# Kernel tuning notes

Hardware: AMD Instinct MI355X
Metric: run time of the kernel (lower is better)

Reference implementation:

```python
import jax, jax.numpy as jnp
import numpy as np

N, E, G = 50000, 150000, 200
D, ED_IN, EH = 320, 15, 32
NB, NT = 3, 9  # conv blocks, edge types


def setup_inputs() -> dict:
    key = jax.random.key(0)
    ks = jax.random.split(key, 16)
    s = 0.02
    return {
        "x": jax.random.normal(ks[0], (N, D), jnp.float32),
        "batch": jnp.sort(jax.random.randint(ks[1], (N,), 0, G)),
        "edge_indices": jax.random.randint(ks[2], (NT, 2, E), 0, N),
        "edge_attrs": jax.random.normal(ks[3], (NT, E, ED_IN), jnp.float32),
        "W1": jax.random.normal(ks[4], (2 * D + ED_IN, EH), jnp.float32) * s,
        "b1": jnp.zeros((EH,), jnp.float32),
        "W2": jax.random.normal(ks[5], (EH, EH), jnp.float32) * s,
        "b2": jnp.zeros((EH,), jnp.float32),
        "Wq": jax.random.normal(ks[6], (NB, NT, D, D), jnp.float32) * s,
        "bq": jnp.zeros((NB, NT, D), jnp.float32),
        "Wk": jax.random.normal(ks[7], (NB, NT, D, D), jnp.float32) * s,
        "bk": jnp.zeros((NB, NT, D), jnp.float32),
        "Wv": jax.random.normal(ks[8], (NB, NT, D, D), jnp.float32) * s,
        "bv": jnp.zeros((NB, NT, D), jnp.float32),
        "We": jax.random.normal(ks[9], (NB, NT, EH, D), jnp.float32) * s,
        "be": jnp.zeros((NB, NT, D), jnp.float32),
        "Ws": jax.random.normal(ks[10], (NB, NT, D, D), jnp.float32) * s,
        "bs": jnp.zeros((NB, NT, D), jnp.float32),
        "gamma": jnp.ones((NB, D), jnp.float32),
        "beta": jnp.zeros((NB, D), jnp.float32),
    }


def _transformer_conv(x, src, dst, ea, Wq, bq, Wk, bk, Wv, bv, We, be, Ws, bs):
    # PyG TransformerConv, heads=1, edge_dim=EH, eval mode (no dropout).
    q = (x @ Wq + bq)[dst]                    # [E, D] query at destination
    e = ea @ We + be                          # [E, D] projected edge attr
    k = (x @ Wk + bk)[src] + e                # [E, D]
    v = (x @ Wv + bv)[src] + e                # [E, D]
    alpha = (q * k).sum(-1) / jnp.sqrt(jnp.float32(D))  # [E]
    amax = jax.ops.segment_max(alpha, dst, num_segments=N)
    amax = jnp.where(jnp.isfinite(amax), amax, 0.0)     # guard empty segments
    ex = jnp.exp(alpha - amax[dst])
    denom = jax.ops.segment_sum(ex, dst, num_segments=N)
    w = ex / (denom[dst] + 1e-16)
    out = jax.ops.segment_sum(w[:, None] * v, dst, num_segments=N)
    return out + x @ Ws + bs                  # root/skip connection


def _graph_layer_norm(x, batch, gamma, beta):
    # PyG gnn.norm.LayerNorm, mode='graph': normalize per graph over nodes+channels.
    cnt = jax.ops.segment_sum(jnp.ones((N,), x.dtype), batch, num_segments=G)
    norm = jnp.maximum(cnt, 1.0) * D          # elements per graph
    mean = jax.ops.segment_sum(x.sum(-1), batch, num_segments=G) / norm
    xc = x - mean[batch][:, None]
    var = jax.ops.segment_sum((xc * xc).sum(-1), batch, num_segments=G) / norm
    out = xc / jnp.sqrt(var + 1e-5)[batch][:, None]
    return out * gamma + beta


def reference(x, batch, edge_indices, edge_attrs, W1, b1, W2, b2,
              Wq, bq, Wk, bk, Wv, bv, We, be, Ws, bs, gamma, beta):
    # Edge MLP preprocessing (uses original node features x).
    new_ea = []
    for t in range(NT):
        src, dst = edge_indices[t, 0], edge_indices[t, 1]
        cat = jnp.concatenate([x[src], x[dst], edge_attrs[t]], axis=-1)  # [E, 655]
        h = jax.nn.leaky_relu(cat @ W1 + b1)
        new_ea.append(h @ W2 + b2)

    h = x
    for b in range(NB):
        acc = jnp.zeros_like(h)
        for t in range(NT):
            src, dst = edge_indices[t, 0], edge_indices[t, 1]
            acc = acc + _transformer_conv(
                h, src, dst, new_ea[t],
                Wq[b, t], bq[b, t], Wk[b, t], bk[b, t], Wv[b, t], bv[b, t],
                We[b, t], be[b, t], Ws[b, t], bs[b, t])
        x_ = jax.nn.leaky_relu(acc / 9.0)
        x_ = _graph_layer_norm(x_, batch, gamma[b], beta[b])
        h = 0.5 * (h + x_)

    return jax.ops.segment_max(h, batch, num_segments=G)  # global max pool [G, D]
```

## Files before the change

### kernel.cpp

```cpp
#include <hip/hip_runtime.h>

#define N_NODES 50000
#define N_EDGE  150000
#define N_GRAPH 200
#define DIM     320
#define EDI     15
#define EH      32
#define NBLK    3
#define NTYP    9
#define NPAD    51200
#define BPT     50
#define QLD     360
#define QCOLS   353
#define NPQ     384
#define BIGCH   448

typedef unsigned short u16;
typedef unsigned int   u32;
typedef __bf16 bf16x8 __attribute__((ext_vector_type(8)));
typedef float  f32x4  __attribute__((ext_vector_type(4)));

__device__ __forceinline__ float b2f(u16 s) {
    u32 u = ((u32)s) << 16;
    return __builtin_bit_cast(float, u);
}
__device__ __forceinline__ float b2f_lo(u32 u) { return __builtin_bit_cast(float, u << 16); }
__device__ __forceinline__ float b2f_hi(u32 u) { return __builtin_bit_cast(float, u & 0xffff0000u); }
__device__ __forceinline__ u16 f2b(float f) {
    u32 u = __builtin_bit_cast(u32, f);
    u = (u + 0x7fffu + ((u >> 16) & 1u)) >> 16;
    return (u16)u;
}

__device__ __forceinline__ void gll16(const u16* g, u32 ldsAddr) {
    u32 m0v = (u32)__builtin_amdgcn_readfirstlane((int)ldsAddr);
    asm volatile("s_mov_b32 m0, %0\n\t"
                 "global_load_lds_dwordx4 %1, off"
                 :: "s"(m0v), "v"((unsigned long long)(size_t)g)
                 : "memory");
}

__global__ __launch_bounds__(256) void gemm_kernel(
    const u16* __restrict__ A, int Mstride,
    const u16* __restrict__ Bst, const float* __restrict__ bias,
    u16* __restrict__ Cb, float* __restrict__ Cf,
    int ldc, int out_cols, int M, int NP, int KQ, int mode,
    int zA, int zB, int zC)
{
    A += (size_t)blockIdx.z * zA;
    Bst += (size_t)blockIdx.z * zB;
    if (Cb) Cb += (size_t)blockIdx.z * zC;
    if (Cf) Cf += (size_t)blockIdx.z * zC;

    const int tid = threadIdx.x;
    const int wave = tid >> 6, lane = tid & 63;

    const int nwg = gridDim.x * gridDim.y;
    const int flat = blockIdx.y * gridDim.x + blockIdx.x;
    const int qq = nwg >> 3, rr = nwg & 7;
    const int xcd = flat & 7, loc = flat >> 3;
    const int swz = (xcd < rr ? xcd * (qq + 1) : rr * (qq + 1) + (xcd - rr) * qq) + loc;
    const int n0 = (swz % gridDim.x) * 128, m0 = (swz / gridDim.x) * 128;

    const int wm = (wave & 1) << 6, wn = (wave >> 1) << 6;
    const int lm = lane & 15, quad = lane >> 4;

    __shared__ uint4 smem[3][2][512];
    const u32 ldsBase = (u32)(size_t)&smem[0][0][0];

    f32x4 acc[4][4] = {};
    const int nIter = KQ >> 2;

    auto stage = [&](int s, int buf) {
        const int c0 = s << 2;
        const u32 bufBase = ldsBase + (u32)buf * 16384u;
#pragma unroll
        for (int u = 0; u < 2; ++u) {
            const int i = wave + (u << 2);
            const int chunk = i >> 1, half = (i & 1) << 6;
            const u16* ga = A + ((size_t)(c0 + chunk) * Mstride + m0 + half + lane) * 8;
            gll16(ga, bufBase + (u32)i * 1024u);
            const u16* gb = Bst + ((size_t)(c0 + chunk) * NP + n0 + half + lane) * 8;
            gll16(gb, bufBase + 8192u + (u32)i * 1024u);
        }
    };

    stage(0, 0);
    if (nIter > 1) {
        stage(1, 1);
        asm volatile("s_waitcnt vmcnt(4)" ::: "memory");
    } else {
        asm volatile("s_waitcnt vmcnt(0)" ::: "memory");
    }
    __syncthreads();

    int bRd = 0, bIss = 2;
    for (int s = 0; s < nIter; ++s) {
        const bool more = (s + 2 < nIter);
        if (more) { stage(s + 2, bIss); bIss = (bIss == 2) ? 0 : bIss + 1; }
        const uint4* aT = &smem[bRd][0][0];
        const uint4* bT = &smem[bRd][1][0];
        bf16x8 af[4], bfr[4];
#pragma unroll
        for (int mi = 0; mi < 4; ++mi)
            af[mi] = __builtin_bit_cast(bf16x8, aT[quad * 128 + wm + mi * 16 + lm]);
#pragma unroll
        for (int ni = 0; ni < 4; ++ni)
            bfr[ni] = __builtin_bit_cast(bf16x8, bT[quad * 128 + wn + ni * 16 + lm]);
#pragma unroll
        for (int mi = 0; mi < 4; ++mi)
#pragma unroll
            for (int ni = 0; ni < 4; ++ni)
                acc[mi][ni] = __builtin_amdgcn_mfma_f32_16x16x32_bf16(af[mi], bfr[ni], acc[mi][ni], 0, 0, 0);
        if (s + 1 < nIter) {
            if (more) asm volatile("s_waitcnt vmcnt(4)" ::: "memory");
            else      asm volatile("s_waitcnt vmcnt(0)" ::: "memory");
            __syncthreads();
        }
        bRd = (bRd == 2) ? 0 : bRd + 1;
    }

#pragma unroll
    for (int mi = 0; mi < 4; ++mi) {
        int row = m0 + wm + mi * 16 + quad * 4;
#pragma unroll
        for (int ni = 0; ni < 4; ++ni) {
            int col = n0 + wn + ni * 16 + lm;
            float bv = bias ? bias[col] : 0.f;
#pragma unroll
            for (int r = 0; r < 4; ++r) {
                int rr2 = row + r;
                if (rr2 < M && col < out_cols) {
                    float v = acc[mi][ni][r] + bv;
                    size_t off = (size_t)rr2 * ldc + col;
                    if (mode == 0)      Cb[off] = f2b(v);
                    else if (mode == 1) Cf[off] = v;
                    else                Cf[off] += v;
                }
            }
        }
    }
}

__global__ void k_convert_x(const float* __restrict__ x, u16* __restrict__ hb,
                            u16* __restrict__ hNode) {
    int i = blockIdx.x * 256 + threadIdx.x;
    if (i >= N_NODES * DIM) return;
    int node = i / DIM, c = i - node * DIM;
    u16 v = f2b(x[i]);
    hb[((size_t)(c >> 3) * N_NODES + node) * 8 + (c & 7)] = v;
    hNode[i] = v;
}

__global__ void k_prep_wT(const float* __restrict__ W, u16* __restrict__ T) {
    int i = blockIdx.x * 256 + threadIdx.x;
    if (i >= 27 * 40 * 320) return;
    int e = i % 320, jq = (i / 320) % 40, bt = i / (320 * 40);
    const float* src = W + ((size_t)bt * 320 + e) * 320 + jq * 8;
    u16 tmp[8];
#pragma unroll
    for (int r = 0; r < 8; ++r) tmp[r] = f2b(src[r]);
    *(uint4*)(&T[(((size_t)bt * 40 + jq) * 320 + e) * 8]) = *(uint4*)tmp;
}

__global__ void k_prep_qkvW(const u16* __restrict__ Mb, u16* __restrict__ Bst) {
    int i = blockIdx.x * 256 + threadIdx.x;
    if (i >= 27 * 40 * NPQ) return;
    int col = i % NPQ, kq = (i / NPQ) % 40, bt = i / (NPQ * 40);
    if (col >= 320 && col < QCOLS) return;
    u16 tmp[8];
    if (col >= QCOLS) {
#pragma unroll
        for (int r = 0; r < 8; ++r) tmp[r] = 0;
    } else {
#pragma unroll
        for (int r = 0; r < 8; ++r)
            tmp[r] = Mb[((size_t)bt * 320 + kq * 8 + r) * 320 + col];
    }
    *(uint4*)(&Bst[(((size_t)bt * 40 + kq) * NPQ + col) * 8]) = *(uint4*)tmp;
}

__global__ __launch_bounds__(256) void k_prep_ext(
    const float* __restrict__ Wq, const float* __restrict__ bq,
    const float* __restrict__ We, const float* __restrict__ be,
    const float* __restrict__ bk,
    u16* __restrict__ Bst, float* __restrict__ biasQkv)
{
    __shared__ float WeL[33 * 321];
    int bt = blockIdx.x, kt = blockIdx.y;
    for (int i = threadIdx.x; i < 33 * 320; i += 256) {
        int r = i / 320, d = i - r * 320;
        WeL[r * 321 + d] = (r < 32) ? We[((size_t)bt * 32 + r) * 320 + d]
                                    : (be[(size_t)bt * 320 + d] + bk[(size_t)bt * 320 + d]);
    }
    __syncthreads();
    if (kt < 10) {
        int k  = kt * 32 + (threadIdx.x >> 3);
        int ct = threadIdx.x & 7;
        const float* wq = Wq + ((size_t)bt * 320 + k) * 320;
        float dot[5] = {0.f, 0.f, 0.f, 0.f, 0.f};
        for (int d = 0; d < 320; ++d) {
            float w = wq[d];
            dot[0] += w * WeL[ct * 321 + d];
            dot[1] += w * WeL[(ct + 8) * 321 + d];
            dot[2] += w * WeL[(ct + 16) * 321 + d];
            dot[3] += w * WeL[(ct + 24) * 321 + d];
            dot[4] += w * WeL[32 * 321 + d];
        }
#pragma unroll
        for (int u = 0; u < 4; ++u)
            Bst[(((size_t)bt * 40 + (k >> 3)) * NPQ + 320 + ct + u * 8) * 8 + (k & 7)] = f2b(dot[u]);
        if (ct == 0)
            Bst[(((size_t)bt * 40 + (k >> 3)) * NPQ + 352) * 8 + (k & 7)] = f2b(dot[4]);
    } else {
        int c = threadIdx.x;
        if (c < 33) {
            const float* b = bq + (size_t)bt * 320;
            float s = 0.f;
            for (int d = 0; d < 320; ++d) s += b[d] * WeL[c * 321 + d];
            biasQkv[bt * NPQ + 320 + c] = s;
        }
    }
}

__global__ __launch_bounds__(256) void k_prep_qkvB(
    const float* __restrict__ Wk, const float* __restrict__ bq,
    float* __restrict__ bias)
{
    int i = blockIdx.x * 256 + threadIdx.x;
    if (i >= 27 * NPQ) return;
    int col = i % NPQ, bt = i / NPQ;
    if (col < 320) {
        const float4* wr = (const float4*)(Wk + ((size_t)bt * 320 + col) * 320);
        const float4* bb = (const float4*)(bq + (size_t)bt * 320);
        float s = 0.f;
        for (int j = 0; j < 80; ++j) {
            float4 a = wr[j], b = bb[j];
            s += a.x * b.x + a.y * b.y + a.z * b.z + a.w * b.w;
        }
        bias[bt * NPQ + col] = s;
    } else if (col >= QCOLS) {
        bias[bt * NPQ + col] = 0.f;
    }
}

__global__ void k_prep_skipB(const float* __restrict__ bs, float* __restrict__ bias) {
    int i = blockIdx.x * 256 + threadIdx.x;
    if (i >= 3 * 384) return;
    int col = i % 384, b = i / 384;
    float v = 0.f;
    if (col < 320)
        for (int t = 0; t < 9; ++t) v += bs[(b * 9 + t) * 320 + col];
    bias[i] = v;
}

__global__ void k_prep_bigB(const float* __restrict__ Ws, const float* __restrict__ Wv,
                            const float* __restrict__ We, const float* __restrict__ be,
                            const float* __restrict__ bv, u16* __restrict__ Bst) {
    int i = blockIdx.x * 256 + threadIdx.x;
    if (i >= 3 * BIGCH * 384) return;
    int col = i % 384, q = (i / 384) % BIGCH, b = i / (384 * BIGCH);
    u16 tmp[8];
#pragma unroll
    for (int r = 0; r < 8; ++r) {
        int k = q * 8 + r;
        float v = 0.f;
        if (col < 320) {
            if (k < 320) {
                for (int t = 0; t < 9; ++t)
                    v += Ws[((size_t)(b * 9 + t) * 320 + k) * 320 + col];
            } else {
                int kk = k - 320, t = kk / 360, kl = kk - t * 360;
                if (t < 9) {
                    int bt = b * 9 + t;
                    if (kl < 320)       v = Wv[((size_t)bt * 320 + kl) * 320 + col];
                    else if (kl < 352)  v = We[((size_t)bt * 32 + (kl - 320)) * 320 + col];
                    else if (kl == 352) v = be[(size_t)bt * 320 + col] + bv[(size_t)bt * 320 + col];
                }
            }
        }
        tmp[r] = f2b(v);
    }
    *(uint4*)(&Bst[(((size_t)b * BIGCH + q) * 384 + col) * 8]) = *(uint4*)tmp;
}

__global__ void k_prep_w1W(const float* __restrict__ W1, u16* __restrict__ Bst) {
    int i = blockIdx.x * 256 + threadIdx.x;
    if (i >= 320 * 128) return;
    int col = i & 127, k = i >> 7;
    float v = 0.f;
    if (col < 32)      v = W1[(size_t)k * 32 + col];
    else if (col < 64) v = W1[(size_t)(320 + k) * 32 + (col - 32)];
    Bst[((size_t)(k >> 3) * 128 + col) * 8 + (k & 7)] = f2b(v);
}

__global__ void k_csr_zero(int* __restrict__ cnt) {
    int i = blockIdx.x * 256 + threadIdx.x;
    if (i < NTYP * NPAD) cnt[i] = 0;
}
__global__ void k_csr_count(const int* __restrict__ eidx, int* __restrict__ cnt) {
    int i = blockIdx.x * 256 + threadIdx.x;
    if (i >= NTYP * N_EDGE) return;
    int t = i / N_EDGE, e = i - t * N_EDGE;
    int dst = eidx[(size_t)(t * 2 + 1) * N_EDGE + e];
    atomicAdd(&cnt[t * NPAD + dst], 1);
}
__global__ __launch_bounds__(1024) void k_csr_scan1(const int* __restrict__ cnt,
                                                    int* __restrict__ rowStart,
                                                    int* __restrict__ blockSum) {
    __shared__ int tmp[1024];
    int t = blockIdx.y, blk = blockIdx.x, tid = threadIdx.x;
    int idx = t * NPAD + blk * 1024 + tid;
    int v = cnt[idx];
    tmp[tid] = v;
    __syncthreads();
    for (int off = 1; off < 1024; off <<= 1) {
        int x = (tid >= off) ? tmp[tid - off] : 0;
        __syncthreads();
        tmp[tid] += x;
        __syncthreads();
    }
    rowStart[idx] = tmp[tid] - v;
    if (tid == 1023) blockSum[t * 64 + blk] = tmp[tid];
}
__global__ void k_csr_scan2(int* __restrict__ blockSum) {
    int t = threadIdx.x;
    if (t >= NTYP) return;
    int run = 0;
    for (int b = 0; b < BPT; ++b) {
        int v = blockSum[t * 64 + b];
        blockSum[t * 64 + b] = run;
        run += v;
    }
}
__global__ void k_csr_scan3(int* __restrict__ rowStart, const int* __restrict__ blockSum,
                            int* __restrict__ cursor) {
    int i = blockIdx.x * 256 + threadIdx.x;
    if (i >= NTYP * NPAD) return;
    int t = i / NPAD, n = i - t * NPAD;
    int v = rowStart[i] + blockSum[t * 64 + (n >> 10)];
    rowStart[i] = v;
    cursor[i] = v;
}
__global__ void k_csr_scatter(const int* __restrict__ eidx, int* __restrict__ cursor,
                              u16* __restrict__ sSrc, int* __restrict__ sEid) {
    int i = blockIdx.x * 256 + threadIdx.x;
    if (i >= NTYP * N_EDGE) return;
    int t = i / N_EDGE, e = i - t * N_EDGE;
    int src = eidx[(size_t)(t * 2) * N_EDGE + e];
    int dst = eidx[(size_t)(t * 2 + 1) * N_EDGE + e];
    int pos = atomicAdd(&cursor[t * NPAD + dst], 1);
    sSrc[(size_t)t * N_EDGE + pos] = (u16)src;
    sEid[(size_t)t * N_EDGE + pos] = e;
}

__global__ __launch_bounds__(256) void k_edge_mlp(
    const u16* __restrict__ Anodes, const int* __restrict__ eidx,
    const float* __restrict__ eattr, const float* __restrict__ W1,
    const float* __restrict__ b1, const float* __restrict__ W2,
    const float* __restrict__ b2, u16* __restrict__ outEa, int t)
{
    __shared__ float w1c[EDI][EH];
    __shared__ float w2s[EH][EH];
    __shared__ float b1s[EH], b2s[EH];
    int tid = threadIdx.x;
    for (int i = tid; i < EDI * EH; i += 256) w1c[i / EH][i % EH] = W1[(640 + i / EH) * EH + (i % EH)];
    for (int i = tid; i < EH * EH; i += 256) w2s[i / EH][i % EH] = W2[i];
    if (tid < EH) { b1s[tid] = b1[tid]; b2s[tid] = b2[tid]; }
    __syncthreads();

    int e = blockIdx.x * 256 + tid;
    if (e >= N_EDGE) return;
    int src = eidx[(size_t)(t * 2) * N_EDGE + e];
    int dst = eidx[(size_t)(t * 2 + 1) * N_EDGE + e];
    const float* eat = eattr + ((size_t)t * N_EDGE + e) * EDI;
    const u16* a1 = Anodes + (size_t)src * 64;
    const u16* a2 = Anodes + (size_t)dst * 64 + 32;

    float h1[EH];
#pragma unroll
    for (int j = 0; j < EH; ++j) h1[j] = b2f(a1[j]) + b2f(a2[j]) + b1s[j];
    for (int i = 0; i < EDI; ++i) {
        float v = eat[i];
#pragma unroll
        for (int j = 0; j < EH; ++j) h1[j] += v * w1c[i][j];
    }
#pragma unroll
    for (int j = 0; j < EH; ++j) h1[j] = h1[j] > 0.f ? h1[j] : 0.01f * h1[j];

    u16* orow = outEa + (size_t)e * EH;
    for (int j = 0; j < EH; ++j) {
        float o = b2s[j];
#pragma unroll
        for (int i = 0; i < EH; ++i) o += h1[i] * w2s[i][j];
        orow[j] = f2b(o);
    }
}

__global__ __launch_bounds__(256) void k_attn(
    const u16* __restrict__ qkv, const u16* __restrict__ hNode,
    const int* __restrict__ rowStart,
    const u16* __restrict__ sSrc, const int* __restrict__ sEid,
    const u16* __restrict__ ea, u16* __restrict__ hA, int cb)
{
    int wave = threadIdx.x >> 6, lane = threadIdx.x & 63;
    int n = blockIdx.x * 4 + wave;
    if (n >= N_NODES) return;
    int eb = rowStart[n], ee = rowStart[n + 1];

    float l = 0.f, as = 0.f;
    float av0 = 0.f, av1 = 0.f, av2 = 0.f, av3 = 0.f, avt = 0.f;

    if (eb != ee) {
        const u16* qrow = qkv + (size_t)n * QLD;
        uint2 qv = *(const uint2*)(qrow + 4 * lane);
        float q40 = b2f_lo(qv.x), q41 = b2f_hi(qv.x);
        float q42 = b2f_lo(qv.y), q43 = b2f_hi(qv.y);
        float q1 = b2f(qrow[256 + lane]);
        float qwl = (lane < 33) ? b2f(qrow[320 + lane]) : 0.f;
        float qwbe = __shfl(qwl, 32, 64);
        float qw = (lane < 32) ? qwl : 0.f;
        const float RS = 0.05590169943749474f;
        float m = -INFINITY;

        int ei = eb;
        for (; ei + 2 <= ee; ei += 2) {
            int s0 = sSrc[ei], s1 = sSrc[ei + 1];
            int id0 = sEid[ei], id1 = sEid[ei + 1];
            const u16* kr0 = hNode + (size_t)s0 * DIM;
            const u16* kr1 = hNode + (size_t)s1 * DIM;
            uint2 k0v = *(const uint2*)(kr0 + 4 * lane);
            uint2 k1v = *(const uint2*)(kr1 + 4 * lane);
            float k00 = b2f_lo(k0v.x), k01 = b2f_hi(k0v.x);
            float k02 = b2f_lo(k0v.y), k03 = b2f_hi(k0v.y);
            float k10 = b2f_lo(k1v.x), k11 = b2f_hi(k1v.x);
            float k12 = b2f_lo(k1v.y), k13 = b2f_hi(k1v.y);
            float k0t = b2f(kr0[256 + lane]);
            float k1t = b2f(kr1[256 + lane]);
            float ea0 = (lane < 32) ? b2f(ea[(size_t)id0 * 32 + lane]) : 0.f;
            float ea1 = (lane < 32) ? b2f(ea[(size_t)id1 * 32 + lane]) : 0.f;
            float d0 = qw * ea0 + q1 * k0t + q40 * k00 + q41 * k01 + q42 * k02 + q43 * k03;
            float d1 = qw * ea1 + q1 * k1t + q40 * k10 + q41 * k11 + q42 * k12 + q43 * k13;
#pragma unroll
            for (int off = 32; off > 0; off >>= 1) {
                d0 += __shfl_xor(d0, off, 64);
                d1 += __shfl_xor(d1, off, 64);
            }
            float a0 = (d0 + qwbe) * RS, a1 = (d1 + qwbe) * RS;
            float mn = fmaxf(m, fmaxf(a0, a1));
            float sc = __expf(m - mn);
            float p0 = __expf(a0 - mn), p1 = __expf(a1 - mn);
            l = l * sc + p0 + p1;
            av0 = av0 * sc + p0 * k00 + p1 * k10;
            av1 = av1 * sc + p0 * k01 + p1 * k11;
            av2 = av2 * sc + p0 * k02 + p1 * k12;
            av3 = av3 * sc + p0 * k03 + p1 * k13;
            avt = avt * sc + p0 * k0t + p1 * k1t;
            as = as * sc + p0 * ea0 + p1 * ea1;
            m = mn;
        }
        if (ei < ee) {
            int s0 = sSrc[ei];
            int id0 = sEid[ei];
            const u16* kr0 = hNode + (size_t)s0 * DIM;
            uint2 k0v = *(const uint2*)(kr0 + 4 * lane);
            float k00 = b2f_lo(k0v.x), k01 = b2f_hi(k0v.x);
            float k02 = b2f_lo(k0v.y), k03 = b2f_hi(k0v.y);
            float k0t = b2f(kr0[256 + lane]);
            float ea0 = (lane < 32) ? b2f(ea[(size_t)id0 * 32 + lane]) : 0.f;
            float d0 = qw * ea0 + q1 * k0t + q40 * k00 + q41 * k01 + q42 * k02 + q43 * k03;
#pragma unroll
            for (int off = 32; off > 0; off >>= 1) d0 += __shfl_xor(d0, off, 64);
            float a0 = (d0 + qwbe) * RS;
            float mn = fmaxf(m, a0);
            float sc = __expf(m - mn), p0 = __expf(a0 - mn);
            l = l * sc + p0;
            av0 = av0 * sc + p0 * k00;
            av1 = av1 * sc + p0 * k01;
            av2 = av2 * sc + p0 * k02;
            av3 = av3 * sc + p0 * k03;
            avt = avt * sc + p0 * k0t;
            as = as * sc + p0 * ea0;
        }
    }

    float inv = (l > 0.f) ? 1.f / l : 0.f;
    u32 w0 = (u32)f2b(av0 * inv) | ((u32)f2b(av1 * inv) << 16);
    u32 w1 = (u32)f2b(av2 * inv) | ((u32)f2b(av3 * inv) << 16);
    uint2 wv; wv.x = w0; wv.y = w1;
    *(uint2*)(hA + ((size_t)(cb + (lane >> 1)) * N_NODES + n) * 8 + (lane & 1) * 4) = wv;
    hA[((size_t)(cb + 32 + (lane >> 3)) * N_NODES + n) * 8 + (lane & 7)] = f2b(avt * inv);
    if (lane < 32) {
        hA[((size_t)(cb + 40 + (lane >> 3)) * N_NODES + n) * 8 + (lane & 7)] = f2b(as * inv);
    } else if (lane == 32) {
        uint4 fz; fz.x = (eb != ee) ? 0x3f80u : 0u; fz.y = 0u; fz.z = 0u; fz.w = 0u;
        *(uint4*)(hA + ((size_t)(cb + 44) * N_NODES + n) * 8) = fz;
    }
}

__device__ __forceinline__ int lowerb(const int* a, int n, int v) {
    int lo = 0, hi = n;
    while (lo < hi) { int mid = (lo + hi) >> 1; if (a[mid] < v) lo = mid + 1; else hi = mid; }
    return lo;
}

__global__ __launch_bounds__(1024) void k_post(
    const float* __restrict__ acc, u16* __restrict__ hb, u16* __restrict__ hNode,
    const int* __restrict__ batch, const float* __restrict__ gamma,
    const float* __restrict__ beta)
{
    int g = blockIdx.x;
    int start = lowerb(batch, N_NODES, g);
    int end   = lowerb(batch, N_NODES, g + 1);
    int cnt = end - start;
    if (cnt == 0) return;
    int i0 = start * DIM, i1 = end * DIM;

    float s = 0.f, ss = 0.f;
    for (int i = i0 + threadIdx.x; i < i1; i += 1024) {
        float v = acc[i] * (1.f / 9.f);
        v = v > 0.f ? v : 0.01f * v;
        s += v; ss += v * v;
    }
    __shared__ float rs[16], rss[16];
#pragma unroll
    for (int off = 32; off > 0; off >>= 1) { s += __shfl_xor(s, off, 64); ss += __shfl_xor(ss, off, 64); }
    int wave = threadIdx.x >> 6, lane = threadIdx.x & 63;
    if (lane == 0) { rs[wave] = s; rss[wave] = ss; }
    __syncthreads();
    if (threadIdx.x == 0) {
        float S = 0.f, SS = 0.f;
        for (int w = 0; w < 16; ++w) { S += rs[w]; SS += rss[w]; }
        float norm = (float)cnt * DIM;
        float mean = S / norm;
        float var = SS / norm - mean * mean;
        rs[0] = mean;
        rss[0] = rsqrtf(var + 1e-5f);
    }
    __syncthreads();
    float mean = rs[0], rsig = rss[0];
    for (int i = i0 + threadIdx.x; i < i1; i += 1024) {
        float v = acc[i] * (1.f / 9.f);
        v = v > 0.f ? v : 0.01f * v;
        int node = i / DIM, c = i - node * DIM;
        float o = (v - mean) * rsig * gamma[c] + beta[c];
        u16 nb = f2b(0.5f * (b2f(hNode[i]) + o));
        hNode[i] = nb;
        hb[((size_t)(c >> 3) * N_NODES + node) * 8 + (c & 7)] = nb;
    }
}

__global__ __launch_bounds__(320) void k_maxpool(
    const u16* __restrict__ hb, const int* __restrict__ batch, float* __restrict__ out)
{
    int g = blockIdx.x, c = threadIdx.x;
    int start = lowerb(batch, N_NODES, g);
    int end   = lowerb(batch, N_NODES, g + 1);
    size_t base = (size_t)(c >> 3) * N_NODES * 8 + (c & 7);
    float m = -INFINITY;
    for (int n = start; n < end; ++n) m = fmaxf(m, b2f(hb[base + (size_t)n * 8]));
    out[(size_t)g * DIM + c] = m;
}

extern "C" void kernel_launch(void* const* d_in, const int* in_sizes, int n_in,
                              void* d_out, int out_size, void* d_ws, size_t ws_size,
                              hipStream_t stream)
{
    (void)in_sizes; (void)n_in; (void)out_size;
    const float* x     = (const float*)d_in[0];
    const int*   batch = (const int*)d_in[1];
    const int*   eidx  = (const int*)d_in[2];
    const float* eattr = (const float*)d_in[3];
    const float* W1 = (const float*)d_in[4];
    const float* b1 = (const float*)d_in[5];
    const float* W2 = (const float*)d_in[6];
    const float* b2 = (const float*)d_in[7];
    const float* Wq = (const float*)d_in[8];
    const float* bq = (const float*)d_in[9];
    const float* Wk = (const float*)d_in[10];
    const float* bk = (const float*)d_in[11];
    const float* Wv = (const float*)d_in[12];
    const float* bv = (const float*)d_in[13];
    const float* We = (const float*)d_in[14];
    const float* be = (const float*)d_in[15];
    const float* Ws = (const float*)d_in[16];
    const float* bs = (const float*)d_in[17];
    const float* gamma = (const float*)d_in[18];
    const float* beta  = (const float*)d_in[19];
    float* out = (float*)d_out;

    auto al = [](size_t b) -> size_t { return (b + 255) & ~(size_t)255; };
    const size_t szOther =
        al((size_t)N_NODES * DIM * 2)
      + al((size_t)N_NODES * DIM * 4)
      + al((size_t)N_NODES * QLD * 2)
      + al((size_t)N_NODES * 64 * 2)
      + al((size_t)27 * 40 * NPQ * 8 * 2)
      + al((size_t)27 * NPQ * 4)
      + al((size_t)3 * BIGCH * 384 * 8 * 2)
      + al((size_t)3 * 384 * 4)
      + al((size_t)40 * 128 * 8 * 2)
      + al((size_t)NTYP * NPAD * 4) * 2
      + al((size_t)NTYP * 64 * 4)
      + al((size_t)NTYP * N_EDGE * 2)
      + al((size_t)NTYP * N_EDGE * 4);
    const size_t hag2 = al((size_t)132 * N_NODES * 8 * 2 + 1024);
    const size_t hag4 = al((size_t)220 * N_NODES * 8 * 2 + 1024);
    const size_t bigB = (size_t)NTYP * N_EDGE * EH * 2;
    const size_t smlB = (size_t)N_EDGE * EH * 2;
    const size_t mar = 1u << 20;
    int nslots, bigEa;
    if      (ws_size >= hag4 + szOther + bigB + mar) { nslots = 4; bigEa = 1; }
    else if (ws_size >= hag2 + szOther + bigB + mar) { nslots = 2; bigEa = 1; }
    else if (ws_size >= hag4 + szOther + smlB + mar) { nslots = 4; bigEa = 0; }
    else                                             { nslots = 2; bigEa = 0; }
    const int hagch = (nslots == 4) ? 220 : 132;

    char* base = (char*)d_ws;
    size_t off = 0;
    auto carve = [&](size_t bytes) -> char* {
        char* r = base + off;
        off += (bytes + 255) & ~(size_t)255;
        return r;
    };
    u16*   hAg     = (u16*)  carve((size_t)hagch * N_NODES * 8 * 2 + 1024);
    u16*   hNode   = (u16*)  carve((size_t)N_NODES * DIM * 2);
    float* acc     = (float*)carve((size_t)N_NODES * DIM * 4);
    u16*   qkv     = (u16*)  carve((size_t)N_NODES * QLD * 2);
    u16*   Anodes  = (u16*)  carve((size_t)N_NODES * 64 * 2);
    u16*   BstQkv  = (u16*)  carve((size_t)27 * 40 * NPQ * 8 * 2);
    float* biasQkv = (float*)carve((size_t)27 * NPQ * 4);
    u16*   BstBig  = (u16*)  carve((size_t)3 * BIGCH * 384 * 8 * 2);
    float* biasSkip= (float*)carve((size_t)3 * 384 * 4);
    u16*   BstW1   = (u16*)  carve((size_t)40 * 128 * 8 * 2);
    int*   cnt     = (int*)  carve((size_t)NTYP * NPAD * 4);
    int*   rowStart= (int*)  carve((size_t)NTYP * NPAD * 4);
    int*   blockSum= (int*)  carve((size_t)NTYP * 64 * 4);
    u16*   sSrc    = (u16*)  carve((size_t)NTYP * N_EDGE * 2);
    int*   sEid    = (int*)  carve((size_t)NTYP * N_EDGE * 4);
    u16*   newEa   = (u16*)  carve(bigEa ? bigB : smlB);

    u16* regionB = hAg + (size_t)40 * N_NODES * 8;
    u16* AqT = regionB;
    u16* BkT = AqT + 27 * 40 * 320 * 8 + 512;
    u16* Mb  = BkT + 27 * 40 * 320 * 8 + 512;

    k_convert_x<<<(N_NODES * DIM + 255) / 256, 256, 0, stream>>>(x, hAg, hNode);
    if (nslots == 2)
        hipMemsetAsync(hAg + (size_t)130 * N_NODES * 8, 0, (size_t)2 * N_NODES * 8 * 2, stream);
    k_prep_wT<<<(27 * 40 * 320 + 255) / 256, 256, 0, stream>>>(Wq, AqT);
    k_prep_wT<<<(27 * 40 * 320 + 255) / 256, 256, 0, stream>>>(Wk, BkT);
    gemm_kernel<<<dim3(3, 3, 27), 256, 0, stream>>>(AqT, 320, BkT, nullptr,
        Mb, nullptr, 320, 320, 320, 320, 40, 0, 102400, 102400, 102400);
    k_prep_qkvW<<<(27 * 40 * NPQ + 255) / 256, 256, 0, stream>>>(Mb, BstQkv);
    k_prep_ext<<<dim3(27, 11), 256, 0, stream>>>(Wq, bq, We, be, bk, BstQkv, biasQkv);
    k_prep_qkvB<<<(27 * NPQ + 255) / 256, 256, 0, stream>>>(Wk, bq, biasQkv);
    k_prep_skipB<<<(3 * 384 + 255) / 256, 256, 0, stream>>>(bs, biasSkip);
    k_prep_bigB<<<(3 * BIGCH * 384 + 255) / 256, 256, 0, stream>>>(Ws, Wv, We, be, bv, BstBig);
    k_prep_w1W<<<(320 * 128 + 255) / 256, 256, 0, stream>>>(W1, BstW1);

    k_csr_zero<<<(NTYP * NPAD + 255) / 256, 256, 0, stream>>>(cnt);
    k_csr_count<<<(NTYP * N_EDGE + 255) / 256, 256, 0, stream>>>(eidx, cnt);
    k_csr_scan1<<<dim3(BPT, NTYP), 1024, 0, stream>>>(cnt, rowStart, blockSum);
    k_csr_scan2<<<1, 64, 0, stream>>>(blockSum);
    k_csr_scan3<<<(NTYP * NPAD + 255) / 256, 256, 0, stream>>>(rowStart, blockSum, cnt);
    k_csr_scatter<<<(NTYP * N_EDGE + 255) / 256, 256, 0, stream>>>(eidx, cnt, sSrc, sEid);

    const int mt = (N_NODES + 127) / 128;
    const int et = (N_EDGE + 255) / 256;
    gemm_kernel<<<dim3(1, mt), 256, 0, stream>>>(hAg, N_NODES, BstW1, nullptr,
        Anodes, nullptr, 64, 64, N_NODES, 128, 40, 0, 0, 0, 0);
    if (bigEa) {
        for (int t = 0; t < NTYP; ++t)
            k_edge_mlp<<<dim3(et), 256, 0, stream>>>(
                Anodes, eidx, eattr, W1, b1, W2, b2, newEa + (size_t)t * N_EDGE * EH, t);
    }

    for (int b = 0; b < NBLK; ++b) {
        for (int t = 0; t < NTYP; ++t) {
            int bt = b * NTYP + t;
            u16* eaT = bigEa ? (newEa + (size_t)t * N_EDGE * EH) : newEa;
            if (!bigEa)
                k_edge_mlp<<<dim3(et), 256, 0, stream>>>(
                    Anodes, eidx, eattr, W1, b1, W2, b2, eaT, t);
            gemm_kernel<<<dim3(3, mt), 256, 0, stream>>>(
                hAg, N_NODES, BstQkv + (size_t)bt * 40 * NPQ * 8, biasQkv + bt * NPQ,
                qkv, nullptr, QLD, QCOLS, N_NODES, NPQ, 40, 0, 0, 0, 0);
            k_attn<<<dim3(N_NODES / 4), 256, 0, stream>>>(
                qkv, hNode, rowStart + t * NPAD, sSrc + (size_t)t * N_EDGE,
                sEid + (size_t)t * N_EDGE, eaT, hAg, 40 + (t % nslots) * 45);
            if (nslots == 2) {
                if (t & 1) {
                    int g = t >> 1;
                    const int gOff2[4] = {0, 130, 220, 310};
                    const int gKQ2[4]  = {132, 92, 92, 92};
                    gemm_kernel<<<dim3(3, mt), 256, 0, stream>>>(
                        (g == 0) ? hAg : regionB, N_NODES,
                        BstBig + ((size_t)b * BIGCH + gOff2[g]) * 384 * 8,
                        (g == 0) ? (biasSkip + b * 384) : nullptr,
                        nullptr, acc, DIM, DIM, N_NODES, 384, gKQ2[g],
                        (g == 0) ? 1 : 2, 0, 0, 0);
                }
            } else {
                if (t == 3)
                    gemm_kernel<<<dim3(3, mt), 256, 0, stream>>>(
                        hAg, N_NODES, BstBig + (size_t)b * BIGCH * 384 * 8,
                        biasSkip + b * 384, nullptr, acc, DIM, DIM, N_NODES,
                        384, 220, 1, 0, 0, 0);
                else if (t == 7)
                    gemm_kernel<<<dim3(3, mt), 256, 0, stream>>>(
                        regionB, N_NODES, BstBig + ((size_t)b * BIGCH + 220) * 384 * 8,
                        nullptr, nullptr, acc, DIM, DIM, N_NODES,
                        384, 180, 2, 0, 0, 0);
            }
        }
        gemm_kernel<<<dim3(3, mt), 256, 0, stream>>>(
            regionB, N_NODES, BstBig + ((size_t)b * BIGCH + 400) * 384 * 8, nullptr,
            nullptr, acc, DIM, DIM, N_NODES, 384, 48, 2, 0, 0, 0);
        k_post<<<N_GRAPH, 1024, 0, stream>>>(acc, hAg, hNode, batch,
                                             gamma + b * DIM, beta + b * DIM);
    }
    k_maxpool<<<N_GRAPH, 320, 0, stream>>>(hAg, batch, out);
}
```

Before: 5.416 ms.

## Shrink GEMM to single-wave 64x64 tiles with barrier-free double buffering

Rewrites the bf16 MFMA GEMM so each workgroup is one wave computing a 64x64 output tile instead of four waves on 128x128. The LDS pipeline goes from three buffers to two and uses only vmcnt/lgkmcnt waits, with no __syncthreads. The next stage is issued only after the fragment reads of the current buffer have completed. Grids are resized to match, e.g. 5 or 6 column tiles, which also cuts wasted padded columns for the 320- and 353-wide outputs. This drops barrier overhead and partial-tile waste and adds many more blocks, at the cost of half the operand reuse per loaded byte and more global/L2 traffic.

Result: slower. 5.917 ms (+9.3%).

```diff
diff --git a/kernel.cpp b/kernel.cpp
--- a/kernel.cpp
+++ b/kernel.cpp
@@ -40,7 +40,7 @@
                  : "memory");
 }
 
-__global__ __launch_bounds__(256) void gemm_kernel(
+__global__ __launch_bounds__(64) void gemm_kernel(
     const u16* __restrict__ A, int Mstride,
     const u16* __restrict__ Bst, const float* __restrict__ bias,
     u16* __restrict__ Cb, float* __restrict__ Cf,
@@ -52,20 +52,18 @@
     if (Cb) Cb += (size_t)blockIdx.z * zC;
     if (Cf) Cf += (size_t)blockIdx.z * zC;
 
-    const int tid = threadIdx.x;
-    const int wave = tid >> 6, lane = tid & 63;
+    const int lane = threadIdx.x;
 
     const int nwg = gridDim.x * gridDim.y;
     const int flat = blockIdx.y * gridDim.x + blockIdx.x;
     const int qq = nwg >> 3, rr = nwg & 7;
     const int xcd = flat & 7, loc = flat >> 3;
     const int swz = (xcd < rr ? xcd * (qq + 1) : rr * (qq + 1) + (xcd - rr) * qq) + loc;
-    const int n0 = (swz % gridDim.x) * 128, m0 = (swz / gridDim.x) * 128;
-
-    const int wm = (wave & 1) << 6, wn = (wave >> 1) << 6;
+    const int n0 = (swz % gridDim.x) * 64, m0 = (swz / gridDim.x) * 64;
+
     const int lm = lane & 15, quad = lane >> 4;
 
-    __shared__ uint4 smem[3][2][512];
+    __shared__ uint4 smem[2][2][256];
     const u32 ldsBase = (u32)(size_t)&smem[0][0][0];
 
     f32x4 acc[4][4] = {};
@@ -73,59 +71,47 @@
 
     auto stage = [&](int s, int buf) {
         const int c0 = s << 2;
-        const u32 bufBase = ldsBase + (u32)buf * 16384u;
-#pragma unroll
-        for (int u = 0; u < 2; ++u) {
-            const int i = wave + (u << 2);
-            const int chunk = i >> 1, half = (i & 1) << 6;
-            const u16* ga = A + ((size_t)(c0 + chunk) * Mstride + m0 + half + lane) * 8;
-            gll16(ga, bufBase + (u32)i * 1024u);
-            const u16* gb = Bst + ((size_t)(c0 + chunk) * NP + n0 + half + lane) * 8;
-            gll16(gb, bufBase + 8192u + (u32)i * 1024u);
+        const u32 bufBase = ldsBase + (u32)buf * 8192u;
+#pragma unroll
+        for (int c = 0; c < 4; ++c) {
+            gll16(A + ((size_t)(c0 + c) * Mstride + m0 + lane) * 8,
+                  bufBase + (u32)c * 1024u);
+            gll16(Bst + ((size_t)(c0 + c) * NP + n0 + lane) * 8,
+                  bufBase + 4096u + (u32)c * 1024u);
         }
     };
 
     stage(0, 0);
-    if (nIter > 1) {
-        stage(1, 1);
-        asm volatile("s_waitcnt vmcnt(4)" ::: "memory");
-    } else {
-        asm volatile("s_waitcnt vmcnt(0)" ::: "memory");
-    }
-    __syncthreads();
-
-    int bRd = 0, bIss = 2;
+    if (nIter > 1) stage(1, 1);
+
     for (int s = 0; s < nIter; ++s) {
-        const bool more = (s + 2 < nIter);
-        if (more) { stage(s + 2, bIss); bIss = (bIss == 2) ? 0 : bIss + 1; }
-        const uint4* aT = &smem[bRd][0][0];
-        const uint4* bT = &smem[bRd][1][0];
+        if (s + 1 < nIter) asm volatile("s_waitcnt vmcnt(8)" ::: "memory");
+        else               asm volatile("s_waitcnt vmcnt(0)" ::: "memory");
+        const uint4* aT = &smem[s & 1][0][0];
+        const uint4* bT = &smem[s & 1][1][0];
         bf16x8 af[4], bfr[4];
 #pragma unroll
         for (int mi = 0; mi < 4; ++mi)
-            af[mi] = __builtin_bit_cast(bf16x8, aT[quad * 128 + wm + mi * 16 + lm]);
+            af[mi] = __builtin_bit_cast(bf16x8, aT[quad * 64 + mi * 16 + lm]);
 #pragma unroll
         for (int ni = 0; ni < 4; ++ni)
-            bfr[ni] = __builtin_bit_cast(bf16x8, bT[quad * 128 + wn + ni * 16 + lm]);
+            bfr[ni] = __builtin_bit_cast(bf16x8, bT[quad * 64 + ni * 16 + lm]);
+        asm volatile("s_waitcnt lgkmcnt(0)" ::: "memory");
+        __builtin_amdgcn_sched_barrier(0);
+        if (s + 2 < nIter) stage(s + 2, s & 1);
 #pragma unroll
         for (int mi = 0; mi < 4; ++mi)
 #pragma unroll
             for (int ni = 0; ni < 4; ++ni)
                 acc[mi][ni] = __builtin_amdgcn_mfma_f32_16x16x32_bf16(af[mi], bfr[ni], acc[mi][ni], 0, 0, 0);
-        if (s + 1 < nIter) {
-            if (more) asm volatile("s_waitcnt vmcnt(4)" ::: "memory");
-            else      asm volatile("s_waitcnt vmcnt(0)" ::: "memory");
-            __syncthreads();
-        }
-        bRd = (bRd == 2) ? 0 : bRd + 1;
     }
 
 #pragma unroll
     for (int mi = 0; mi < 4; ++mi) {
-        int row = m0 + wm + mi * 16 + quad * 4;
+        int row = m0 + mi * 16 + quad * 4;
 #pragma unroll
         for (int ni = 0; ni < 4; ++ni) {
-            int col = n0 + wn + ni * 16 + lm;
+            int col = n0 + ni * 16 + lm;
             float bv = bias ? bias[col] : 0.f;
 #pragma unroll
             for (int r = 0; r < 4; ++r) {
@@ -650,7 +636,7 @@
         hipMemsetAsync(hAg + (size_t)130 * N_NODES * 8, 0, (size_t)2 * N_NODES * 8 * 2, stream);
     k_prep_wT<<<(27 * 40 * 320 + 255) / 256, 256, 0, stream>>>(Wq, AqT);
     k_prep_wT<<<(27 * 40 * 320 + 255) / 256, 256, 0, stream>>>(Wk, BkT);
-    gemm_kernel<<<dim3(3, 3, 27), 256, 0, stream>>>(AqT, 320, BkT, nullptr,
+    gemm_kernel<<<dim3(5, 5, 27), 64, 0, stream>>>(AqT, 320, BkT, nullptr,
         Mb, nullptr, 320, 320, 320, 320, 40, 0, 102400, 102400, 102400);
     k_prep_qkvW<<<(27 * 40 * NPQ + 255) / 256, 256, 0, stream>>>(Mb, BstQkv);
     k_prep_ext<<<dim3(27, 11), 256, 0, stream>>>(Wq, bq, We, be, bk, BstQkv, biasQkv);
@@ -666,9 +652,9 @@
     k_csr_scan3<<<(NTYP * NPAD + 255) / 256, 256, 0, stream>>>(rowStart, blockSum, cnt);
     k_csr_scatter<<<(NTYP * N_EDGE + 255) / 256, 256, 0, stream>>>(eidx, cnt, sSrc, sEid);
 
-    const int mt = (N_NODES + 127) / 128;
+    const int mt = (N_NODES + 63) / 64;
     const int et = (N_EDGE + 255) / 256;
-    gemm_kernel<<<dim3(1, mt), 256, 0, stream>>>(hAg, N_NODES, BstW1, nullptr,
+    gemm_kernel<<<dim3(1, mt), 64, 0, stream>>>(hAg, N_NODES, BstW1, nullptr,
         Anodes, nullptr, 64, 64, N_NODES, 128, 40, 0, 0, 0, 0);
     if (bigEa) {
         for (int t = 0; t < NTYP; ++t)
@@ -683,7 +669,7 @@
             if (!bigEa)
                 k_edge_mlp<<<dim3(et), 256, 0, stream>>>(
                     Anodes, eidx, eattr, W1, b1, W2, b2, eaT, t);
-            gemm_kernel<<<dim3(3, mt), 256, 0, stream>>>(
+            gemm_kernel<<<dim3(6, mt), 64, 0, stream>>>(
                 hAg, N_NODES, BstQkv + (size_t)bt * 40 * NPQ * 8, biasQkv + bt * NPQ,
                 qkv, nullptr, QLD, QCOLS, N_NODES, NPQ, 40, 0, 0, 0, 0);
             k_attn<<<dim3(N_NODES / 4), 256, 0, stream>>>(
@@ -694,7 +680,7 @@
                     int g = t >> 1;
                     const int gOff2[4] = {0, 130, 220, 310};
                     const int gKQ2[4]  = {132, 92, 92, 92};
-                    gemm_kernel<<<dim3(3, mt), 256, 0, stream>>>(
+                    gemm_kernel<<<dim3(5, mt), 64, 0, stream>>>(
                         (g == 0) ? hAg : regionB, N_NODES,
                         BstBig + ((size_t)b * BIGCH + gOff2[g]) * 384 * 8,
                         (g == 0) ? (biasSkip + b * 384) : nullptr,
@@ -703,18 +689,18 @@
                 }
             } else {
                 if (t == 3)
-                    gemm_kernel<<<dim3(3, mt), 256, 0, stream>>>(
+                    gemm_kernel<<<dim3(5, mt), 64, 0, stream>>>(
                         hAg, N_NODES, BstBig + (size_t)b * BIGCH * 384 * 8,
                         biasSkip + b * 384, nullptr, acc, DIM, DIM, N_NODES,
                         384, 220, 1, 0, 0, 0);
                 else if (t == 7)
-                    gemm_kernel<<<dim3(3, mt), 256, 0, stream>>>(
+                    gemm_kernel<<<dim3(5, mt), 64, 0, stream>>>(
                         regionB, N_NODES, BstBig + ((size_t)b * BIGCH + 220) * 384 * 8,
                         nullptr, nullptr, acc, DIM, DIM, N_NODES,
                         384, 180, 2, 0, 0, 0);
             }
         }
-        gemm_kernel<<<dim3(3, mt), 256, 0, stream>>>(
+        gemm_kernel<<<dim3(5, mt), 64, 0, stream>>>(
             regionB, N_NODES, BstBig + ((size_t)b * BIGCH + 400) * 384 * 8, nullptr,
             nullptr, acc, DIM, DIM, N_NODES, 384, 48, 2, 0, 0, 0);
         k_post<<<N_GRAPH, 1024, 0, stream>>>(acc, hAg, hNode, batch,
```
